# Performance work log

Measured on AMD Instinct MI355X. Metric: run time of the kernel, lower is better.

Reference implementation:

```python
import jax, jax.numpy as jnp
import numpy as np

# dims (see shape_source)
N = 100000          # num_ent
E = 400000          # num edges
B = 2048            # batch of (sub, rel) queries
INIT_DIM = 100
UFD = 100           # user_fe_dim
ENT_DIM = INIT_DIM + 3 * UFD   # feature_method='concat' -> 400
H = 2               # attention heads
D = 64              # per-head dim
GCN = H * D         # gcn_dim = embed_dim = 128 (gcn_layer == 1)
NUM_REL = 50
NR2 = 2 * NUM_REL


def setup_inputs() -> dict:
    key = jax.random.key(0)
    ks = jax.random.split(key, 17)
    inp = {}
    # constructor / forward int tensors
    inp["edge_index"] = jax.random.randint(ks[0], (2, E), 0, N, dtype=jnp.int32)
    inp["edge_type"] = jax.random.randint(ks[1], (E,), 0, NR2, dtype=jnp.int32)
    inp["edge_type_p"] = jax.random.randint(ks[2], (E,), 0, NR2, dtype=jnp.int32)
    inp["ent_feature"] = jax.random.randint(ks[3], (N, 3), 0, 3, dtype=jnp.int32)
    inp["sub"] = jax.random.randint(ks[4], (B,), 0, N, dtype=jnp.int32)
    inp["rel"] = jax.random.randint(ks[5], (B,), 0, NR2, dtype=jnp.int32)
    inp["relp"] = jax.random.randint(ks[6], (B,), 0, NR2, dtype=jnp.int32)
    # learned parameters
    s = 0.02
    inp["id_embed"] = jax.random.normal(ks[7], (N, INIT_DIM), jnp.float32) * s
    inp["gender_tab"] = jax.random.normal(ks[8], (3, UFD), jnp.float32) * s
    inp["age_tab"] = jax.random.normal(ks[9], (9, UFD), jnp.float32) * s
    inp["level_tab"] = jax.random.normal(ks[10], (11, UFD), jnp.float32) * s
    inp["init_rel"] = jax.random.normal(ks[11], (NR2, ENT_DIM), jnp.float32) * s
    inp["W"] = jax.random.normal(ks[12], (ENT_DIM, H * D), jnp.float32) * 0.05
    inp["Wr"] = jax.random.normal(ks[13], (ENT_DIM, H * D), jnp.float32) * 0.05
    inp["att_src"] = jax.random.normal(ks[14], (H, D), jnp.float32) * 0.05
    inp["att_dst"] = jax.random.normal(ks[15], (H, D), jnp.float32) * 0.05
    inp["Wrel"] = jax.random.normal(ks[16], (ENT_DIM, GCN), jnp.float32) * 0.05
    return inp


def _segment_softmax(logits, seg, num_segments):
    # logits: [E, H], seg: [E] destination node ids
    m = jax.ops.segment_max(logits, seg, num_segments=num_segments)
    ex = jnp.exp(logits - m[seg])
    den = jax.ops.segment_sum(ex, seg, num_segments=num_segments)
    return ex / (den[seg] + 1e-16)


def _rghat_conv(x, rel_emb, edge_index, edge_type, W, Wr, att_src, att_dst, Wrel):
    # relational multi-head graph attention (RGHATConv)
    n = x.shape[0]
    h = (x @ W).reshape(n, H, D)                       # [N,H,D] projected nodes
    r_proj = (rel_emb @ Wr).reshape(-1, H, D)          # [R,H,D]
    src, dst = edge_index[0], edge_index[1]
    msg = h[src] + r_proj[edge_type]                   # [E,H,D] edge messages
    logits = jax.nn.leaky_relu(
        jnp.sum(msg * att_src, axis=-1) + jnp.sum(h[dst] * att_dst, axis=-1),
        negative_slope=0.2,
    )                                                  # [E,H]
    alpha = _segment_softmax(logits, dst, n)           # per-destination softmax
    out = jax.ops.segment_sum(alpha[..., None] * msg, dst, num_segments=n)
    out = jnp.tanh(out.reshape(n, H * D))              # [N,GCN]
    r_out = rel_emb @ Wrel                             # [R,GCN]
    return out, r_out


def reference(edge_index, edge_type, edge_type_p, ent_feature, sub, rel, relp,
              id_embed, gender_tab, age_tab, level_tab, init_rel,
              W, Wr, att_src, att_dst, Wrel):
    # feature_method == 'concat': gather per-node feature embeddings and concat
    x1 = gender_tab[ent_feature[:, 0]]
    x2 = age_tab[ent_feature[:, 1]]
    x3 = level_tab[ent_feature[:, 2]]
    init_embed = jnp.concatenate([id_embed, x1, x2, x3], axis=1)  # [N, ENT_DIM]
    # single conv layer (gcn_layer == 1); dropouts are identity in eval
    x, r = _rghat_conv(init_embed, init_rel, edge_index, edge_type,
                       W, Wr, att_src, att_dst, Wrel)
    sub_emb = x[sub]                                   # index_select gather
    # add_parent_rel == False -> r returned whole (relp unused)
    return (sub_emb, r, x)
```

## Files before the change

kernel.cpp:

```cpp
#include <hip/hip_runtime.h>
#include <hip/hip_bf16.h>
#include <hip/hip_fp16.h>

#define N_NODES 100000
#define E_EDGES 400000
#define B_SUB 2048
#define INIT_DIM 100
#define UFD 100
#define ENT_DIM 400
#define GCN 128
#define NR2 100
#define KPAD 416
#define NCH 13
#define CHK 32
#define CAP 64

typedef __attribute__((ext_vector_type(8))) short shortx8;
typedef __attribute__((ext_vector_type(4))) float floatx4;

#define OUT_R_OFF ((long)B_SUB * GCN)
#define OUT_X_OFF ((long)(B_SUB + NR2) * GCN)

__device__ __forceinline__ unsigned short f2b(float f) {
    unsigned u = __float_as_uint(f);
    u += 0x7fffu + ((u >> 16) & 1u);
    return (unsigned short)(u >> 16);
}
__device__ __forceinline__ unsigned pk2(float x, float y) {
    return (unsigned)f2b(x) | ((unsigned)f2b(y) << 16);
}
__device__ __forceinline__ unsigned cvtpk2(float x, float y) {
    unsigned r;
    asm("v_cvt_pk_bf16_f32 %0, %1, %2" : "=v"(r) : "v"(x), "v"(y));
    return r;
}
__device__ __forceinline__ float blo(unsigned u) { return __uint_as_float(u << 16); }
__device__ __forceinline__ float bhi(unsigned u) { return __uint_as_float(u & 0xFFFF0000u); }

__device__ __forceinline__ float fast_tanh(float x) {
    float e2 = __expf(2.f * x);
    return 1.f - 2.f / (e2 + 1.f);
}

__global__ void wt_kernel(const float* __restrict__ W, unsigned short* __restrict__ Wt,
                          int* __restrict__ cursor) {
    int idx = blockIdx.x * 256 + threadIdx.x;
    if (idx < GCN * KPAD) {
        int n = idx & 127, k = idx >> 7;
        unsigned short o = 0;
        if (k < ENT_DIM) o = f2b(W[(long)k * GCN + n]);
        Wt[(long)n * KPAD + k] = o;
    }
    if (idx < N_NODES) cursor[idx] = 0;
}

__global__ __launch_bounds__(256) void rel_kernel(
        const float* __restrict__ init_rel, const float* __restrict__ Wr,
        const float* __restrict__ Wrel, const float* __restrict__ att_src,
        unsigned* __restrict__ rp_b, float* __restrict__ rproj_att,
        float* __restrict__ out_r) {
    int rel = blockIdx.x;
    int t = threadIdx.x;
    int tx = t & 127, kh = t >> 7;
    __shared__ float rl[ENT_DIM];
    __shared__ float p1[2][128], p2[2][128];
    __shared__ float accbuf[128];
    for (int k = t; k < ENT_DIM; k += 256) rl[k] = init_rel[(long)rel * ENT_DIM + k];
    __syncthreads();
    float a1 = 0.f, a2 = 0.f;
    {
        const float* wr = Wr + (long)(kh * 200) * GCN + tx;
        const float* wl = Wrel + (long)(kh * 200) * GCN + tx;
        const float* rv = rl + kh * 200;
#pragma unroll 8
        for (int k = 0; k < 200; ++k) {
            float v = rv[k];
            a1 += v * wr[(long)k * GCN];
            a2 += v * wl[(long)k * GCN];
        }
    }
    p1[kh][tx] = a1;
    p2[kh][tx] = a2;
    __syncthreads();
    if (t < 128) {
        float acc1 = p1[0][tx] + p1[1][tx];
        float acc2 = p2[0][tx] + p2[1][tx];
        out_r[rel * GCN + tx] = acc2;
        accbuf[tx] = acc1;
        int head = tx >> 6, d = tx & 63;
        float v = acc1 * att_src[head * 64 + d];
        for (int off = 32; off > 0; off >>= 1) v += __shfl_down(v, off, 64);
        if (d == 0) rproj_att[rel * 2 + head] = v;
    }
    __syncthreads();
    if (t < 64) rp_b[rel * 64 + t] = pk2(accbuf[t], accbuf[t + 64]);
}

__global__ __launch_bounds__(256) void hgemm_kernel(
        const float* __restrict__ id_embed, const float* __restrict__ gtab,
        const float* __restrict__ atab, const float* __restrict__ ltab,
        const int* __restrict__ ent_feature, const unsigned short* __restrict__ Wt,
        const float* __restrict__ att_src, const float* __restrict__ att_dst,
        unsigned* __restrict__ h_b, float* __restrict__ hsrc_att, float* __restrict__ hdst_att) {
    __shared__ __align__(16) unsigned short Bs[2][128 * CHK];

    int t = threadIdx.x;
    int w = t >> 6, lane = t & 63, quad = lane >> 4, l16 = lane & 15;
    int n0 = blockIdx.x * 128;

    int nrow0 = n0 + w * 16 + l16;
    int nc0 = nrow0 < N_NODES ? nrow0 : N_NODES - 1;
    int nrow1 = nrow0 + 64;
    int nc1 = nrow1 < N_NODES ? nrow1 : N_NODES - 1;
    const float* pid0 = id_embed + (long)nc0 * INIT_DIM;
    const float* pg0  = gtab + ent_feature[nc0 * 3] * UFD;
    const float* pa0  = atab + ent_feature[nc0 * 3 + 1] * UFD;
    const float* pl0  = ltab + ent_feature[nc0 * 3 + 2] * UFD;
    const float* pid1 = id_embed + (long)nc1 * INIT_DIM;
    const float* pg1  = gtab + ent_feature[nc1 * 3] * UFD;
    const float* pa1  = atab + ent_feature[nc1 * 3 + 1] * UFD;
    const float* pl1  = ltab + ent_feature[nc1 * 3 + 2] * UFD;

    int cB = t >> 2;
    int lB8 = ((t & 3) ^ ((t >> 3) & 3)) * 8;
    const unsigned short* bsrc0 = Wt + (long)cB * KPAD + lB8;
    const unsigned short* bsrc1 = Wt + (long)(64 + cB) * KPAD + lB8;

#define SEG0(kg_) ((kg_) < 100 ? pid0 + (kg_) : \
                   (kg_) < 200 ? pg0 + ((kg_) - 100) : \
                   (kg_) < 300 ? pa0 + ((kg_) - 200) : \
                   (kg_) < 400 ? pl0 + ((kg_) - 300) : pid0)
#define SEG1(kg_) ((kg_) < 100 ? pid1 + (kg_) : \
                   (kg_) < 200 ? pg1 + ((kg_) - 100) : \
                   (kg_) < 300 ? pa1 + ((kg_) - 200) : \
                   (kg_) < 400 ? pl1 + ((kg_) - 300) : pid1)

#define STAGE(ch_, bi_) { \
    __builtin_amdgcn_global_load_lds( \
        (const __attribute__((address_space(1))) unsigned*)(bsrc0 + (ch_) * CHK), \
        (__attribute__((address_space(3))) unsigned*)((char*)&Bs[bi_][0] + w * 1024), 16, 0, 0); \
    __builtin_amdgcn_global_load_lds( \
        (const __attribute__((address_space(1))) unsigned*)(bsrc1 + (ch_) * CHK), \
        (__attribute__((address_space(3))) unsigned*)((char*)&Bs[bi_][0] + 4096 + w * 1024), 16, 0, 0); \
}

    floatx4 acc0[8], acc1[8];
#pragma unroll
    for (int c = 0; c < 8; ++c) {
        acc0[c] = (floatx4){0.f, 0.f, 0.f, 0.f};
        acc1[c] = (floatx4){0.f, 0.f, 0.f, 0.f};
    }

    int qB = quad ^ ((l16 >> 1) & 3);

    STAGE(0, 0);
    float4 va0 = *(const float4*)SEG0(quad * 8);
    float4 vb0 = *(const float4*)SEG0(quad * 8 + 4);
    float4 va1 = *(const float4*)SEG1(quad * 8);
    float4 vb1 = *(const float4*)SEG1(quad * 8 + 4);

#pragma unroll
    for (int ch = 0; ch < NCH; ++ch) {
        __syncthreads();
        if (ch + 1 < NCH) STAGE(ch + 1, (ch & 1) ^ 1);
        uint4 u0, u1;
        u0.x = cvtpk2(va0.x, va0.y); u0.y = cvtpk2(va0.z, va0.w);
        u0.z = cvtpk2(vb0.x, vb0.y); u0.w = cvtpk2(vb0.z, vb0.w);
        u1.x = cvtpk2(va1.x, va1.y); u1.y = cvtpk2(va1.z, va1.w);
        u1.z = cvtpk2(vb1.x, vb1.y); u1.w = cvtpk2(vb1.z, vb1.w);
        shortx8 af0 = *(shortx8*)&u0;
        shortx8 af1 = *(shortx8*)&u1;
        if (ch + 1 < NCH) {
            int kg = (ch + 1) * CHK + quad * 8;
            va0 = *(const float4*)SEG0(kg);
            vb0 = *(const float4*)SEG0(kg + 4);
            va1 = *(const float4*)SEG1(kg);
            vb1 = *(const float4*)SEG1(kg + 4);
        }
#pragma unroll
        for (int c = 0; c < 8; ++c) {
            shortx8 b_ = *(const shortx8*)(&Bs[ch & 1][0] + (c * 16 + l16) * CHK + qB * 8);
            acc0[c] = __builtin_amdgcn_mfma_f32_16x16x32_bf16(af0, b_, acc0[c], 0, 0, 0);
            acc1[c] = __builtin_amdgcn_mfma_f32_16x16x32_bf16(af1, b_, acc1[c], 0, 0, 0);
        }
    }
#undef STAGE
#undef SEG0
#undef SEG1

    float attS_r[8], attD_r[8];
#pragma unroll
    for (int c = 0; c < 8; ++c) {
        attS_r[c] = att_src[c * 16 + l16];
        attD_r[c] = att_dst[c * 16 + l16];
    }
#define EPILOG(accA, rowoff_) { \
    int baseRow = n0 + (rowoff_) + w * 16 + quad * 4; \
    _Pragma("unroll") for (int i = 0; i < 4; ++i) { \
        int node = baseRow + i; \
        bool ok = node < N_NODES; \
        _Pragma("unroll") for (int c = 0; c < 4; ++c) \
            if (ok) h_b[(long)node * 64 + c * 16 + l16] = cvtpk2(accA[c][i], accA[c + 4][i]); \
        float s0 = 0.f, s1 = 0.f, d0 = 0.f, d1 = 0.f; \
        _Pragma("unroll") for (int c = 0; c < 8; ++c) { \
            float v = accA[c][i]; \
            if (c < 4) { s0 += v * attS_r[c]; d0 += v * attD_r[c]; } \
            else       { s1 += v * attS_r[c]; d1 += v * attD_r[c]; } \
        } \
        _Pragma("unroll") for (int m = 1; m < 16; m <<= 1) { \
            s0 += __shfl_xor(s0, m, 64); \
            s1 += __shfl_xor(s1, m, 64); \
            d0 += __shfl_xor(d0, m, 64); \
            d1 += __shfl_xor(d1, m, 64); \
        } \
        if (ok && l16 == 0) { \
            *(float2*)&hsrc_att[node * 2] = make_float2(s0, s1); \
            *(float2*)&hdst_att[node * 2] = make_float2(d0, d1); \
        } \
    } }
    EPILOG(acc0, 0)
    EPILOG(acc1, 64)
#undef EPILOG
}

__global__ void fill_kernel(const int* __restrict__ edge_index, const int* __restrict__ edge_type,
                            int* __restrict__ cursor,
                            const float2* __restrict__ hsrc2, const float2* __restrict__ rpa2,
                            const float2* __restrict__ hdst2,
                            uint2* __restrict__ ebuf) {
    int e = blockIdx.x * blockDim.x + threadIdx.x;
    if (e >= E_EDGES) return;
    int src = edge_index[e];
    int dst = edge_index[E_EDGES + e];
    int et = edge_type[e];
    float2 hs = hsrc2[src];
    float2 ra = rpa2[et];
    float2 hd = hdst2[dst];
    float x0 = hs.x + ra.x + hd.x;
    float x1 = hs.y + ra.y + hd.y;
    x0 = x0 > 0.f ? x0 : 0.2f * x0;
    x1 = x1 > 0.f ? x1 : 0.2f * x1;
    __half2 hh = __floats2half2_rn(__expf(x0), __expf(x1));
    union { __half2 h; unsigned u; } cv; cv.h = hh;
    int pos = atomicAdd(&cursor[dst], 1);
    if (pos < CAP)
        ebuf[(long)dst * CAP + pos] = make_uint2(((unsigned)et << 17) | (unsigned)src, cv.u);
}

__global__ __launch_bounds__(256) void agg_kernel(
        const int* __restrict__ cursor, const uint2* __restrict__ ebuf,
        const unsigned* __restrict__ h_b, const unsigned* __restrict__ rp_b,
        float* __restrict__ out_x) {
    int w = threadIdx.x >> 6, l = threadIdx.x & 63;
    int dstA = (blockIdx.x * 4 + w) * 2;
    int dstB = dstA + 1;
    const uint4* baseA = (const uint4*)(ebuf + (long)dstA * CAP);
    const uint4* baseB = (const uint4*)(ebuf + (long)dstB * CAP);
    uint4 qA = baseA[0];
    uint4 qB = baseB[0];
    int cntA = cursor[dstA]; if (cntA > CAP) cntA = CAP;
    int cntB = cursor[dstB]; if (cntB > CAP) cntB = CAP;
    int jm = cntA > cntB ? cntA : cntB;

    float aA0 = 0.f, aA1 = 0.f, dA0 = 0.f, dA1 = 0.f;
    float aB0 = 0.f, aB1 = 0.f, dB0 = 0.f, dB1 = 0.f;

    for (int j = 0; j < jm; j += 2) {
        unsigned iA0 = j     < cntA ? qA.x : 0u, eA0u = j     < cntA ? qA.y : 0u;
        unsigned iA1 = j + 1 < cntA ? qA.z : 0u, eA1u = j + 1 < cntA ? qA.w : 0u;
        unsigned iB0 = j     < cntB ? qB.x : 0u, eB0u = j     < cntB ? qB.y : 0u;
        unsigned iB1 = j + 1 < cntB ? qB.z : 0u, eB1u = j + 1 < cntB ? qB.w : 0u;
        if (j + 2 < jm) {
            qA = baseA[(j >> 1) + 1];
            qB = baseB[(j >> 1) + 1];
        }
        unsigned hbA0 = h_b[(long)(iA0 & 0x1FFFF) * 64 + l];
        unsigned hbA1 = h_b[(long)(iA1 & 0x1FFFF) * 64 + l];
        unsigned hbB0 = h_b[(long)(iB0 & 0x1FFFF) * 64 + l];
        unsigned hbB1 = h_b[(long)(iB1 & 0x1FFFF) * 64 + l];
        unsigned rbA0 = rp_b[(iA0 >> 17) * 64 + l];
        unsigned rbA1 = rp_b[(iA1 >> 17) * 64 + l];
        unsigned rbB0 = rp_b[(iB0 >> 17) * 64 + l];
        unsigned rbB1 = rp_b[(iB1 >> 17) * 64 + l];
        union { __half2 h; unsigned u; } cA0, cA1, cB0, cB1;
        cA0.u = eA0u; cA1.u = eA1u; cB0.u = eB0u; cB1.u = eB1u;
        float2 fA0 = __half22float2(cA0.h), fA1 = __half22float2(cA1.h);
        float2 fB0 = __half22float2(cB0.h), fB1 = __half22float2(cB1.h);
        aA0 += fA0.x * (blo(hbA0) + blo(rbA0)) + fA1.x * (blo(hbA1) + blo(rbA1));
        aA1 += fA0.y * (bhi(hbA0) + bhi(rbA0)) + fA1.y * (bhi(hbA1) + bhi(rbA1));
        aB0 += fB0.x * (blo(hbB0) + blo(rbB0)) + fB1.x * (blo(hbB1) + blo(rbB1));
        aB1 += fB0.y * (bhi(hbB0) + bhi(rbB0)) + fB1.y * (bhi(hbB1) + bhi(rbB1));
        dA0 += fA0.x + fA1.x;  dA1 += fA0.y + fA1.y;
        dB0 += fB0.x + fB1.x;  dB1 += fB0.y + fB1.y;
    }
    float rA0 = __builtin_amdgcn_rcpf(dA0 + 1e-16f);
    float rA1 = __builtin_amdgcn_rcpf(dA1 + 1e-16f);
    float rB0 = __builtin_amdgcn_rcpf(dB0 + 1e-16f);
    float rB1 = __builtin_amdgcn_rcpf(dB1 + 1e-16f);
    __builtin_nontemporal_store(fast_tanh(aA0 * rA0), &out_x[(long)dstA * GCN + l]);
    __builtin_nontemporal_store(fast_tanh(aA1 * rA1), &out_x[(long)dstA * GCN + 64 + l]);
    __builtin_nontemporal_store(fast_tanh(aB0 * rB0), &out_x[(long)dstB * GCN + l]);
    __builtin_nontemporal_store(fast_tanh(aB1 * rB1), &out_x[(long)dstB * GCN + 64 + l]);
}

__global__ void gather_kernel(const int* __restrict__ sub, const float* __restrict__ out_x,
                              float* __restrict__ out_sub) {
    int idx = blockIdx.x * blockDim.x + threadIdx.x;
    if (idx >= B_SUB * GCN) return;
    int b = idx >> 7, d = idx & 127;
    out_sub[idx] = out_x[(long)sub[b] * GCN + d];
}

extern "C" void kernel_launch(void* const* d_in, const int* in_sizes, int n_in,
                              void* d_out, int out_size, void* d_ws, size_t ws_size,
                              hipStream_t stream) {
    const int* edge_index = (const int*)d_in[0];
    const int* edge_type  = (const int*)d_in[1];
    const int* ent_feature = (const int*)d_in[3];
    const int* sub = (const int*)d_in[4];
    const float* id_embed = (const float*)d_in[7];
    const float* gtab = (const float*)d_in[8];
    const float* atab = (const float*)d_in[9];
    const float* ltab = (const float*)d_in[10];
    const float* init_rel = (const float*)d_in[11];
    const float* W = (const float*)d_in[12];
    const float* Wr = (const float*)d_in[13];
    const float* att_src = (const float*)d_in[14];
    const float* att_dst = (const float*)d_in[15];
    const float* Wrel = (const float*)d_in[16];

    char* ws = (char*)d_ws;
    unsigned* h_b = (unsigned*)ws;                          ws += (long)N_NODES * 64 * 4;
    unsigned* rp_b = (unsigned*)ws;                         ws += (long)NR2 * 64 * 4;
    float* rproj_att = (float*)ws;                          ws += NR2 * 2 * 4;
    float* hsrc_att = (float*)ws;                           ws += (long)N_NODES * 2 * 4;
    float* hdst_att = (float*)ws;                           ws += (long)N_NODES * 2 * 4;
    unsigned short* Wt = (unsigned short*)ws;               ws += (long)GCN * KPAD * 2;
    int* cursor = (int*)ws;                                 ws += (long)N_NODES * 4;
    uint2* ebuf = (uint2*)ws;                               ws += (long)N_NODES * CAP * 8;

    float* out = (float*)d_out;
    float* out_sub = out;
    float* out_r = out + OUT_R_OFF;
    float* out_x = out + OUT_X_OFF;

    const int NB = (N_NODES + 255) / 256;

    wt_kernel<<<NB, 256, 0, stream>>>(W, Wt, cursor);
    rel_kernel<<<NR2, 256, 0, stream>>>(init_rel, Wr, Wrel, att_src, rp_b, rproj_att, out_r);
    hgemm_kernel<<<(N_NODES + 127) / 128, 256, 0, stream>>>(id_embed, gtab, atab, ltab,
                                                            ent_feature, Wt, att_src, att_dst,
                                                            h_b, hsrc_att, hdst_att);
    fill_kernel<<<(E_EDGES + 255) / 256, 256, 0, stream>>>(edge_index, edge_type, cursor,
                                                           (const float2*)hsrc_att,
                                                           (const float2*)rproj_att,
                                                           (const float2*)hdst_att, ebuf);
    agg_kernel<<<N_NODES / 8, 256, 0, stream>>>(cursor, ebuf, h_b, rp_b, out_x);
    gather_kernel<<<(B_SUB * GCN + 255) / 256, 256, 0, stream>>>(sub, out_x, out_sub);
}
```

Before: 231.4 us.

## Process four destinations per wave, stage relation table in LDS, two edges per fill thread

```diff
diff --git a/kernel.cpp b/kernel.cpp
--- a/kernel.cpp
+++ b/kernel.cpp
@@ -228,79 +228,110 @@
                             const float2* __restrict__ hsrc2, const float2* __restrict__ rpa2,
                             const float2* __restrict__ hdst2,
                             uint2* __restrict__ ebuf) {
-    int e = blockIdx.x * blockDim.x + threadIdx.x;
-    if (e >= E_EDGES) return;
-    int src = edge_index[e];
-    int dst = edge_index[E_EDGES + e];
-    int et = edge_type[e];
-    float2 hs = hsrc2[src];
-    float2 ra = rpa2[et];
-    float2 hd = hdst2[dst];
-    float x0 = hs.x + ra.x + hd.x;
-    float x1 = hs.y + ra.y + hd.y;
-    x0 = x0 > 0.f ? x0 : 0.2f * x0;
-    x1 = x1 > 0.f ? x1 : 0.2f * x1;
-    __half2 hh = __floats2half2_rn(__expf(x0), __expf(x1));
-    union { __half2 h; unsigned u; } cv; cv.h = hh;
-    int pos = atomicAdd(&cursor[dst], 1);
-    if (pos < CAP)
-        ebuf[(long)dst * CAP + pos] = make_uint2(((unsigned)et << 17) | (unsigned)src, cv.u);
+    int e0 = blockIdx.x * 512 + threadIdx.x;
+    int e1 = e0 + 256;
+    bool ok0 = e0 < E_EDGES, ok1 = e1 < E_EDGES;
+    int s0i = 0, d0i = 0, t0i = 0, s1i = 0, d1i = 0, t1i = 0;
+    if (ok0) { s0i = edge_index[e0]; d0i = edge_index[E_EDGES + e0]; t0i = edge_type[e0]; }
+    if (ok1) { s1i = edge_index[e1]; d1i = edge_index[E_EDGES + e1]; t1i = edge_type[e1]; }
+    float2 hs0 = hsrc2[s0i], hd0 = hdst2[d0i], ra0 = rpa2[t0i];
+    float2 hs1 = hsrc2[s1i], hd1 = hdst2[d1i], ra1 = rpa2[t1i];
+    if (ok0) {
+        float x0 = hs0.x + ra0.x + hd0.x;
+        float x1 = hs0.y + ra0.y + hd0.y;
+        x0 = x0 > 0.f ? x0 : 0.2f * x0;
+        x1 = x1 > 0.f ? x1 : 0.2f * x1;
+        __half2 hh = __floats2half2_rn(__expf(x0), __expf(x1));
+        union { __half2 h; unsigned u; } cv; cv.h = hh;
+        int pos = atomicAdd(&cursor[d0i], 1);
+        if (pos < CAP)
+            ebuf[(long)d0i * CAP + pos] = make_uint2(((unsigned)t0i << 17) | (unsigned)s0i, cv.u);
+    }
+    if (ok1) {
+        float x0 = hs1.x + ra1.x + hd1.x;
+        float x1 = hs1.y + ra1.y + hd1.y;
+        x0 = x0 > 0.f ? x0 : 0.2f * x0;
+        x1 = x1 > 0.f ? x1 : 0.2f * x1;
+        __half2 hh = __floats2half2_rn(__expf(x0), __expf(x1));
+        union { __half2 h; unsigned u; } cv; cv.h = hh;
+        int pos = atomicAdd(&cursor[d1i], 1);
+        if (pos < CAP)
+            ebuf[(long)d1i * CAP + pos] = make_uint2(((unsigned)t1i << 17) | (unsigned)s1i, cv.u);
+    }
 }
 
 __global__ __launch_bounds__(256) void agg_kernel(
         const int* __restrict__ cursor, const uint2* __restrict__ ebuf,
         const unsigned* __restrict__ h_b, const unsigned* __restrict__ rp_b,
         float* __restrict__ out_x) {
-    int w = threadIdx.x >> 6, l = threadIdx.x & 63;
-    int dstA = (blockIdx.x * 4 + w) * 2;
-    int dstB = dstA + 1;
-    const uint4* baseA = (const uint4*)(ebuf + (long)dstA * CAP);
-    const uint4* baseB = (const uint4*)(ebuf + (long)dstB * CAP);
-    uint4 qA = baseA[0];
-    uint4 qB = baseB[0];
-    int cntA = cursor[dstA]; if (cntA > CAP) cntA = CAP;
-    int cntB = cursor[dstB]; if (cntB > CAP) cntB = CAP;
-    int jm = cntA > cntB ? cntA : cntB;
-
-    float aA0 = 0.f, aA1 = 0.f, dA0 = 0.f, dA1 = 0.f;
-    float aB0 = 0.f, aB1 = 0.f, dB0 = 0.f, dB1 = 0.f;
+    __shared__ unsigned rp_s[NR2 * 64];
+    int t = threadIdx.x;
+    for (int i = t; i < NR2 * 64; i += 256) rp_s[i] = rp_b[i];
+    int w = t >> 6, l = t & 63;
+    int dstBase = (blockIdx.x * 4 + w) * 4;
+    const uint4* base[4];
+    uint4 q[4];
+    int cnt[4];
+#pragma unroll
+    for (int d = 0; d < 4; ++d) {
+        base[d] = (const uint4*)(ebuf + (long)(dstBase + d) * CAP);
+        q[d] = base[d][0];
+    }
+#pragma unroll
+    for (int d = 0; d < 4; ++d) {
+        cnt[d] = cursor[dstBase + d];
+        if (cnt[d] > CAP) cnt[d] = CAP;
+    }
+    int jm = max(max(cnt[0], cnt[1]), max(cnt[2], cnt[3]));
+    __syncthreads();
+
+    float a0[4] = {0.f, 0.f, 0.f, 0.f}, a1[4] = {0.f, 0.f, 0.f, 0.f};
+    float dn0[4] = {0.f, 0.f, 0.f, 0.f}, dn1[4] = {0.f, 0.f, 0.f, 0.f};
 
     for (int j = 0; j < jm; j += 2) {
-        unsigned iA0 = j     < cntA ? qA.x : 0u, eA0u = j     < cntA ? qA.y : 0u;
-        unsigned iA1 = j + 1 < cntA ? qA.z : 0u, eA1u = j + 1 < cntA ? qA.w : 0u;
-        unsigned iB0 = j     < cntB ? qB.x : 0u, eB0u = j     < cntB ? qB.y : 0u;
-        unsigned iB1 = j + 1 < cntB ? qB.z : 0u, eB1u = j + 1 < cntB ? qB.w : 0u;
+        unsigned i0[4], e0u[4], i1[4], e1u[4];
+#pragma unroll
+        for (int d = 0; d < 4; ++d) {
+            i0[d]  = j     < cnt[d] ? q[d].x : 0u;
+            e0u[d] = j     < cnt[d] ? q[d].y : 0u;
+            i1[d]  = j + 1 < cnt[d] ? q[d].z : 0u;
+            e1u[d] = j + 1 < cnt[d] ? q[d].w : 0u;
+        }
         if (j + 2 < jm) {
-            qA = baseA[(j >> 1) + 1];
-            qB = baseB[(j >> 1) + 1];
-        }
-        unsigned hbA0 = h_b[(long)(iA0 & 0x1FFFF) * 64 + l];
-        unsigned hbA1 = h_b[(long)(iA1 & 0x1FFFF) * 64 + l];
-        unsigned hbB0 = h_b[(long)(iB0 & 0x1FFFF) * 64 + l];
-        unsigned hbB1 = h_b[(long)(iB1 & 0x1FFFF) * 64 + l];
-        unsigned rbA0 = rp_b[(iA0 >> 17) * 64 + l];
-        unsigned rbA1 = rp_b[(iA1 >> 17) * 64 + l];
-        unsigned rbB0 = rp_b[(iB0 >> 17) * 64 + l];
-        unsigned rbB1 = rp_b[(iB1 >> 17) * 64 + l];
-        union { __half2 h; unsigned u; } cA0, cA1, cB0, cB1;
-        cA0.u = eA0u; cA1.u = eA1u; cB0.u = eB0u; cB1.u = eB1u;
-        float2 fA0 = __half22float2(cA0.h), fA1 = __half22float2(cA1.h);
-        float2 fB0 = __half22float2(cB0.h), fB1 = __half22float2(cB1.h);
-        aA0 += fA0.x * (blo(hbA0) + blo(rbA0)) + fA1.x * (blo(hbA1) + blo(rbA1));
-        aA1 += fA0.y * (bhi(hbA0) + bhi(rbA0)) + fA1.y * (bhi(hbA1) + bhi(rbA1));
-        aB0 += fB0.x * (blo(hbB0) + blo(rbB0)) + fB1.x * (blo(hbB1) + blo(rbB1));
-        aB1 += fB0.y * (bhi(hbB0) + bhi(rbB0)) + fB1.y * (bhi(hbB1) + bhi(rbB1));
-        dA0 += fA0.x + fA1.x;  dA1 += fA0.y + fA1.y;
-        dB0 += fB0.x + fB1.x;  dB1 += fB0.y + fB1.y;
-    }
-    float rA0 = __builtin_amdgcn_rcpf(dA0 + 1e-16f);
-    float rA1 = __builtin_amdgcn_rcpf(dA1 + 1e-16f);
-    float rB0 = __builtin_amdgcn_rcpf(dB0 + 1e-16f);
-    float rB1 = __builtin_amdgcn_rcpf(dB1 + 1e-16f);
-    __builtin_nontemporal_store(fast_tanh(aA0 * rA0), &out_x[(long)dstA * GCN + l]);
-    __builtin_nontemporal_store(fast_tanh(aA1 * rA1), &out_x[(long)dstA * GCN + 64 + l]);
-    __builtin_nontemporal_store(fast_tanh(aB0 * rB0), &out_x[(long)dstB * GCN + l]);
-    __builtin_nontemporal_store(fast_tanh(aB1 * rB1), &out_x[(long)dstB * GCN + 64 + l]);
+#pragma unroll
+            for (int d = 0; d < 4; ++d) q[d] = base[d][(j >> 1) + 1];
+        }
+        unsigned hb0[4], hb1[4], rb0[4], rb1[4];
+#pragma unroll
+        for (int d = 0; d < 4; ++d) {
+            hb0[d] = h_b[(long)(i0[d] & 0x1FFFF) * 64 + l];
+            hb1[d] = h_b[(long)(i1[d] & 0x1FFFF) * 64 + l];
+        }
+#pragma unroll
+        for (int d = 0; d < 4; ++d) {
+            rb0[d] = rp_s[(i0[d] >> 17) * 64 + l];
+            rb1[d] = rp_s[(i1[d] >> 17) * 64 + l];
+        }
+#pragma unroll
+        for (int d = 0; d < 4; ++d) {
+            union { __half2 h; unsigned u; } c0, c1;
+            c0.u = e0u[d]; c1.u = e1u[d];
+            float2 f0 = __half22float2(c0.h), f1 = __half22float2(c1.h);
+            a0[d] += f0.x * (blo(hb0[d]) + blo(rb0[d])) + f1.x * (blo(hb1[d]) + blo(rb1[d]));
+            a1[d] += f0.y * (bhi(hb0[d]) + bhi(rb0[d])) + f1.y * (bhi(hb1[d]) + bhi(rb1[d]));
+            dn0[d] += f0.x + f1.x;
+            dn1[d] += f0.y + f1.y;
+        }
+    }
+#pragma unroll
+    for (int d = 0; d < 4; ++d) {
+        float r0 = __builtin_amdgcn_rcpf(dn0[d] + 1e-16f);
+        float r1 = __builtin_amdgcn_rcpf(dn1[d] + 1e-16f);
+        __builtin_nontemporal_store(fast_tanh(a0[d] * r0),
+                                    &out_x[(long)(dstBase + d) * GCN + l]);
+        __builtin_nontemporal_store(fast_tanh(a1[d] * r1),
+                                    &out_x[(long)(dstBase + d) * GCN + 64 + l]);
+    }
 }
 
 __global__ void gather_kernel(const int* __restrict__ sub, const float* __restrict__ out_x,
@@ -351,10 +382,10 @@
     hgemm_kernel<<<(N_NODES + 127) / 128, 256, 0, stream>>>(id_embed, gtab, atab, ltab,
                                                             ent_feature, Wt, att_src, att_dst,
                                                             h_b, hsrc_att, hdst_att);
-    fill_kernel<<<(E_EDGES + 255) / 256, 256, 0, stream>>>(edge_index, edge_type, cursor,
+    fill_kernel<<<(E_EDGES + 511) / 512, 256, 0, stream>>>(edge_index, edge_type, cursor,
                                                            (const float2*)hsrc_att,
                                                            (const float2*)rproj_att,
                                                            (const float2*)hdst_att, ebuf);
-    agg_kernel<<<N_NODES / 8, 256, 0, stream>>>(cursor, ebuf, h_b, rp_b, out_x);
+    agg_kernel<<<N_NODES / 16, 256, 0, stream>>>(cursor, ebuf, h_b, rp_b, out_x);
     gather_kernel<<<(B_SUB * GCN + 255) / 256, 256, 0, stream>>>(sub, out_x, out_sub);
 }
```

Result: no change. 232.2 us (+0.4%).
